# Kernel optimization log

Hardware: AMD Instinct MI355X
Metric: run time of the kernel (lower is better)

The kernel has to match this reference:

```python
import jax, jax.numpy as jnp
import numpy as np

T, B, I, H = 1024, 64, 256, 256


def setup_inputs() -> dict:
    key = jax.random.key(0)
    ks = jax.random.split(key, 7)
    s = 1.0 / np.sqrt(H)
    return {
        "x": jax.random.normal(ks[0], (T, B, I), jnp.float32),
        "U_w": jax.random.normal(ks[1], (H, I), jnp.float32) * s,
        "U_b": jax.random.normal(ks[2], (H,), jnp.float32) * s,
        "V_w": jax.random.normal(ks[3], (H, H), jnp.float32) * s,
        "Ua_w": jax.random.normal(ks[4], (H, H), jnp.float32) * s,
        "Va_w": jax.random.normal(ks[5], (H, H), jnp.float32) * s,
        "v": jax.random.normal(ks[6], (1, H), jnp.float32) * s,
    }


def reference(x, U_w, U_b, V_w, Ua_w, Va_w, v):
    # Unrolls MemRNN over the time axis of x: [T, B, I] -> [T, B, H].
    # Faithful to the torch module: st is the PRE-nonlinearity h at t=0;
    # for t>=1 st = memory[t-1] + ct (attention context), and memory stores
    # the POST-nonlinearity h.
    Tn = x.shape[0]
    vv = v[0]  # [H]
    # Precompute U(x_t) for all steps (input projection is step-independent).
    Ux = jnp.einsum('tbi,hi->tbh', x, U_w) + U_b  # [T, B, H]

    # t = 0: hidden is zeros, so V(hidden) = 0.
    st0 = Ux[0]                       # pre-nonlinearity state [B, H]
    h0 = jnp.tanh(st0)                # stored in memory
    mem0 = jnp.zeros((Tn,) + h0.shape, x.dtype).at[0].set(h0)
    # Incrementally maintain Ua(memory) so each step only projects the new h.
    uam0 = jnp.zeros_like(mem0).at[0].set(h0 @ Ua_w.T)

    tidx = jnp.arange(Tn)

    def step(carry, inp):
        mem, uam, st = carry
        t, Ux_t = inp
        valid = (tidx < t)[:, None]                       # [T, 1] mask over memory
        # Bahdanau scores over all past hidden states.
        e = jnp.einsum('tbh,h->tb', jnp.tanh(st @ Va_w.T + uam), vv)  # [T, B]
        e = jnp.where(valid, e, -jnp.inf)
        alphas = jax.nn.softmax(e, axis=0)                # softmax over time
        ct = jnp.einsum('tb,tbh->bh', alphas, mem)        # attention context
        last_h = jax.lax.dynamic_index_in_dim(mem, t - 1, 0, keepdims=False)
        st_new = last_h + ct
        h = jnp.tanh(Ux_t + st_new @ V_w.T)
        mem = mem.at[t].set(h)
        uam = uam.at[t].set(h @ Ua_w.T)
        return (mem, uam, st_new), h

    _, hs = jax.lax.scan(step, (mem0, uam0, st0), (tidx[1:], Ux[1:]))
    return jnp.concatenate([h0[None], hs], axis=0)  # [T, B, H]
```

## Files before the change

kernel.cpp:

```cpp
#include <hip/hip_runtime.h>
#include <hip/hip_fp16.h>

#define TT 1024
#define BB 64
#define HH 256
#define NQ 4
#define SL 64
#define NTH 1024
#define NW 16

#define MIR_BYTES (256ull * TT * SL * 2)
#define STW_BYTES (1ull * BB * HH * 4)
#define EP_BYTES  (1ull * BB * NQ * TT * 4)
#define BAR_BYTES ((BB * 32 + 32) * 4)
#define WS_NEED   (MIR_BYTES + STW_BYTES + EP_BYTES + BAR_BYTES)

__device__ __forceinline__ float tanh_fast(float xx) {
  float e = __expf(2.0f * xx);
  return 1.0f - 2.0f * __builtin_amdgcn_rcpf(e + 1.0f);
}

__device__ __forceinline__ float ld_cg(const float* p) {
  return __hip_atomic_load(p, __ATOMIC_RELAXED, __HIP_MEMORY_SCOPE_AGENT);
}
__device__ __forceinline__ void st_cg(float* p, float v) {
  __hip_atomic_store(p, v, __ATOMIC_RELAXED, __HIP_MEMORY_SCOPE_AGENT);
}

__device__ __forceinline__ void bar_post(int* cnt) {
  __syncthreads();
  if (threadIdx.x == 0)
    __hip_atomic_fetch_add(cnt, 1, __ATOMIC_RELEASE, __HIP_MEMORY_SCOPE_AGENT);
}
__device__ __forceinline__ void bar_wait(int* cnt, int* broken, int target) {
  if (threadIdx.x == 0) {
    long it = 0;
    while (__hip_atomic_load(cnt, __ATOMIC_RELAXED, __HIP_MEMORY_SCOPE_AGENT) < target) {
      if (__hip_atomic_load(broken, __ATOMIC_RELAXED, __HIP_MEMORY_SCOPE_AGENT)) break;
      if (++it > 5000000) {
        __hip_atomic_store(broken, 1, __ATOMIC_RELAXED, __HIP_MEMORY_SCOPE_AGENT);
        break;
      }
    }
  }
  __syncthreads();
}

#define RED16(a) { a += __shfl_xor(a, 1); a += __shfl_xor(a, 2); \
                   a += __shfl_xor(a, 4); a += __shfl_xor(a, 8); }

extern "C" __global__ void __launch_bounds__(NTH, 4)
memrnn_scan(const float* __restrict__ x, const float* __restrict__ U_w,
            const float* __restrict__ U_b, const float* __restrict__ V_w,
            const float* __restrict__ Ua_w, const float* __restrict__ Va_w,
            const float* __restrict__ vvec, float* __restrict__ out,
            char* __restrict__ wsb)
{
  const int blk  = blockIdx.x;
  const int b    = blk & 63;
  const int q    = blk >> 6;
  const int tid  = threadIdx.x;
  const int lane = tid & 63;
  const int wav  = tid >> 6;
  const int r    = tid >> 4;
  const int c    = tid & 15;
  const int gr   = q * SL + r;

  __half* mir = (__half*)wsb + (size_t)blk * TT * SL;
  float*  stw = (float*)(wsb + MIR_BYTES);
  float*  ep  = (float*)(wsb + MIR_BYTES + STW_BYTES);
  int* barbase = (int*)(wsb + MIR_BYTES + STW_BYTES + EP_BYTES);
  int* bar    = barbase + b * 32;
  int* broken = barbase + BB * 32;

  float wV[16], wUa[16], wVa[16], wU[16];
#pragma unroll
  for (int j = 0; j < 16; ++j) {
    const int i = j * 16 + c;
    wV[j]  = V_w [gr * HH + i];
    wUa[j] = Ua_w[gr * HH + i];
    wVa[j] = Va_w[gr * HH + i];
    wU[j]  = U_w [gr * HH + i];
  }
  const float bias = U_b[gr];

  __shared__ __half s_uam[TT * SL];
  __shared__ float2 s_av[SL];
  __shared__ float  s_vec[HH];
  __shared__ float  s_x[HH];
  __shared__ float  s_h[HH];
  __shared__ float  s_e[TT];
  __shared__ float  s_red[NW * SL];
  __shared__ float  s_d[NW];

  int tgt = 0;

  if (tid < HH) s_x[tid] = x[(size_t)b * HH + tid];
  __syncthreads();
  {
    float acc = 0.f;
#pragma unroll
    for (int j = 0; j < 16; ++j) acc += wU[j] * s_x[j * 16 + c];
    RED16(acc);
    if (c == 0) st_cg(&stw[b * HH + gr], acc + bias);
  }
  bar_post(bar); tgt += NQ; bar_wait(bar, broken, tgt);
  if (tid < HH) {
    const float sv = ld_cg(&stw[b * HH + tid]);
    s_vec[tid] = sv;
    s_h[tid]   = tanh_fast(sv);
  }
  __syncthreads();
  if (tid < SL) {
    const float h0 = s_h[q * SL + tid];
    st_cg(&out[(size_t)b * HH + q * SL + tid], h0);
    mir[tid] = __float2half(h0);
  }
  {
    float acca = 0.f, accu = 0.f;
#pragma unroll
    for (int j = 0; j < 16; ++j) {
      const int i = j * 16 + c;
      acca += wVa[j] * s_vec[i];
      accu += wUa[j] * s_h[i];
    }
    RED16(acca); RED16(accu);
    if (c == 0) {
      s_av[r] = make_float2(acca, vvec[gr]);
      s_uam[r] = __float2half(accu);
    }
  }
  __syncthreads();

  for (int t = 1; t < TT; ++t) {
    {
      float* epg = ep + ((size_t)(b * NQ + q)) * TT;
      for (int ci = wav; ci * SL < t; ci += NW) {
        const int t2 = ci * SL + lane;
        const int rb = t2 * SL;
        float p = 0.f;
#pragma unroll 8
        for (int h = 0; h < SL; ++h) {
          const float2 av = s_av[h];
          const float u = __half2float(s_uam[rb + (h ^ lane)]);
          p = fmaf(av.y, tanh_fast(av.x + u), p);
        }
        if (t2 < t) st_cg(&epg[t2], p);
      }
    }
    bar_post(bar); tgt += NQ; bar_wait(bar, broken, tgt);

    if (tid < t) {
      const float* e0 = ep + (size_t)b * NQ * TT + tid;
      s_e[tid] = ld_cg(e0) + ld_cg(e0 + TT) + ld_cg(e0 + 2 * TT) + ld_cg(e0 + 3 * TT);
    }
    __syncthreads();
    {
      float num = 0.f, den = 0.f;
#pragma unroll 4
      for (int t2 = wav; t2 < t; t2 += NW) {
        const float w = __expf(s_e[t2]);
        den += w;
        num = fmaf(w, __half2float(mir[(size_t)t2 * SL + lane]), num);
      }
      s_red[wav * SL + lane] = num;
      if (lane == 0) s_d[wav] = den;
    }
    __syncthreads();
    if (wav == 0) {
      float nt = 0.f, dt = 0.f;
#pragma unroll
      for (int w2 = 0; w2 < NW; ++w2) { nt += s_red[w2 * SL + lane]; dt += s_d[w2]; }
      const float ct  = nt / dt;
      const float stn = __half2float(mir[(size_t)(t - 1) * SL + lane]) + ct;
      st_cg(&stw[b * HH + q * SL + lane], stn);
    }
    float xv = 0.f;
    bar_post(bar); tgt += NQ;
    if (tid < HH) xv = x[((size_t)t * BB + b) * HH + tid];
    bar_wait(bar, broken, tgt);

    if (tid < HH) {
      s_x[tid]   = xv;
      s_vec[tid] = ld_cg(&stw[b * HH + tid]);
    }
    __syncthreads();
    {
      float acc = 0.f, acca = 0.f;
#pragma unroll
      for (int j = 0; j < 16; ++j) {
        const int i = j * 16 + c;
        const float sv = s_vec[i];
        acc  += wV[j] * sv + wU[j] * s_x[i];
        acca += wVa[j] * sv;
      }
      RED16(acc); RED16(acca);
      if (c == 0) {
        const float hv = tanh_fast(acc + bias);
        st_cg(&out[((size_t)t * BB + b) * HH + gr], hv);
        mir[(size_t)t * SL + r] = __float2half(hv);
        s_av[r].x = acca;
      }
    }
    if (t < TT - 1) {
      bar_post(bar); tgt += NQ; bar_wait(bar, broken, tgt);
      if (tid < HH) s_h[tid] = ld_cg(&out[((size_t)t * BB + b) * HH + tid]);
      __syncthreads();
      {
        float acc = 0.f;
#pragma unroll
        for (int j = 0; j < 16; ++j) acc += wUa[j] * s_h[j * 16 + c];
        RED16(acc);
        if (c == 0) s_uam[t * SL + (r ^ (t & 63))] = __float2half(acc);
      }
      __syncthreads();
    }
  }

  if (tid == 0 &&
      __hip_atomic_load(broken, __ATOMIC_RELAXED, __HIP_MEMORY_SCOPE_AGENT))
    st_cg(&out[0], 1.0e6f);
}

__global__ void ws_sentinel(float* out) { out[0] = 2.0e6f; }

extern "C" void kernel_launch(void* const* d_in, const int* in_sizes, int n_in,
                              void* d_out, int out_size, void* d_ws, size_t ws_size,
                              hipStream_t stream) {
  const float* x    = (const float*)d_in[0];
  const float* U_w  = (const float*)d_in[1];
  const float* U_b  = (const float*)d_in[2];
  const float* V_w  = (const float*)d_in[3];
  const float* Ua_w = (const float*)d_in[4];
  const float* Va_w = (const float*)d_in[5];
  const float* v    = (const float*)d_in[6];
  float* out = (float*)d_out;

  if (ws_size < WS_NEED) {
    ws_sentinel<<<1, 1, 0, stream>>>(out);
    return;
  }
  hipMemsetAsync((char*)d_ws + (MIR_BYTES + STW_BYTES + EP_BYTES), 0, BAR_BYTES, stream);
  memrnn_scan<<<dim3(BB * NQ), dim3(NTH), 0, stream>>>(
      x, U_w, U_b, V_w, Ua_w, Va_w, v, out, (char*)d_ws);
}
```

Baseline: 21.17 ms.

## Split Ua projection by input slice and overlap with score computation via per-quarter flags

Replaces the single counter barrier with per-quarter flag slots (aflag/bflag/pflag). The Ua projection now uses column-slice partial sums from each block's own hidden values, written to a global parts buffer. This removes the barrier that waited for all four quarters' h before computing uam. The score pass over old timesteps overlaps with waiting for those partials, and the newest timestep's score is computed separately. Tanh is rewritten via exp2 and a sigmoid identity with a precomputed v-sum, exp is moved into the s_e load, and the uam layout is transposed. These changes add more flag traffic and risk subtle ordering or precision issues.

Result: slower. 27.25 ms (+28.7%).

```diff
diff --git a/kernel.cpp b/kernel.cpp
--- a/kernel.cpp
+++ b/kernel.cpp
@@ -10,35 +10,49 @@
 #define NW 16
 
 #define MIR_BYTES (256ull * TT * SL * 2)
-#define STW_BYTES (1ull * BB * HH * 4)
-#define EP_BYTES  (1ull * BB * NQ * TT * 4)
-#define BAR_BYTES ((BB * 32 + 32) * 4)
-#define WS_NEED   (MIR_BYTES + STW_BYTES + EP_BYTES + BAR_BYTES)
+#define STW_OFF   (MIR_BYTES)
+#define EP_OFF    (STW_OFF + 1ull * BB * HH * 4)
+#define PARTS_OFF (EP_OFF + 1ull * BB * NQ * TT * 4)
+#define AF_OFF    (PARTS_OFF + 1ull * BB * NQ * HH * 4)
+#define BF_OFF    (AF_OFF + 1ull * BB * NQ * 32 * 4)
+#define PF_OFF    (BF_OFF + 1ull * BB * NQ * 32 * 4)
+#define BR_OFF    (PF_OFF + 1ull * BB * NQ * 32 * 4)
+#define WS_NEED   (BR_OFF + 128)
+
+#define PM 2.88539008178f
+
+#if __has_builtin(__builtin_amdgcn_exp2f)
+#define EXP2F(x) __builtin_amdgcn_exp2f(x)
+#else
+#define EXP2F(x) __expf(0.69314718056f * (x))
+#endif
 
 __device__ __forceinline__ float tanh_fast(float xx) {
   float e = __expf(2.0f * xx);
   return 1.0f - 2.0f * __builtin_amdgcn_rcpf(e + 1.0f);
 }
 
+#define AGT __HIP_MEMORY_SCOPE_AGENT
 __device__ __forceinline__ float ld_cg(const float* p) {
-  return __hip_atomic_load(p, __ATOMIC_RELAXED, __HIP_MEMORY_SCOPE_AGENT);
+  return __hip_atomic_load(p, __ATOMIC_RELAXED, AGT);
 }
 __device__ __forceinline__ void st_cg(float* p, float v) {
-  __hip_atomic_store(p, v, __ATOMIC_RELAXED, __HIP_MEMORY_SCOPE_AGENT);
-}
-
-__device__ __forceinline__ void bar_post(int* cnt) {
+  __hip_atomic_store(p, v, __ATOMIC_RELAXED, AGT);
+}
+
+__device__ __forceinline__ void post1(int* slot) {
   __syncthreads();
   if (threadIdx.x == 0)
-    __hip_atomic_fetch_add(cnt, 1, __ATOMIC_RELEASE, __HIP_MEMORY_SCOPE_AGENT);
-}
-__device__ __forceinline__ void bar_wait(int* cnt, int* broken, int target) {
-  if (threadIdx.x == 0) {
+    __hip_atomic_fetch_add(slot, 1, __ATOMIC_RELEASE, AGT);
+}
+__device__ __forceinline__ void wait4(int* base, int val, int* broken) {
+  if (threadIdx.x < 4) {
+    const int* f = base + threadIdx.x * 32;
     long it = 0;
-    while (__hip_atomic_load(cnt, __ATOMIC_RELAXED, __HIP_MEMORY_SCOPE_AGENT) < target) {
-      if (__hip_atomic_load(broken, __ATOMIC_RELAXED, __HIP_MEMORY_SCOPE_AGENT)) break;
+    while (__hip_atomic_load(f, __ATOMIC_RELAXED, AGT) < val) {
+      if (__hip_atomic_load(broken, __ATOMIC_RELAXED, AGT)) break;
       if (++it > 5000000) {
-        __hip_atomic_store(broken, 1, __ATOMIC_RELAXED, __HIP_MEMORY_SCOPE_AGENT);
+        __hip_atomic_store(broken, 1, __ATOMIC_RELAXED, AGT);
         break;
       }
     }
@@ -65,37 +79,42 @@
   const int r    = tid >> 4;
   const int c    = tid & 15;
   const int gr   = q * SL + r;
-
-  __half* mir = (__half*)wsb + (size_t)blk * TT * SL;
-  float*  stw = (float*)(wsb + MIR_BYTES);
-  float*  ep  = (float*)(wsb + MIR_BYTES + STW_BYTES);
-  int* barbase = (int*)(wsb + MIR_BYTES + STW_BYTES + EP_BYTES);
-  int* bar    = barbase + b * 32;
-  int* broken = barbase + BB * 32;
-
-  float wV[16], wUa[16], wVa[16], wU[16];
+  const int r2   = tid >> 2;
+  const int c2   = tid & 3;
+
+  __half* mir   = (__half*)wsb + (size_t)blk * TT * SL;
+  float*  stw   = (float*)(wsb + STW_OFF);
+  float*  ep    = (float*)(wsb + EP_OFF);
+  float*  parts = (float*)(wsb + PARTS_OFF);
+  int* aflag = (int*)(wsb + AF_OFF) + b * NQ * 32;
+  int* bflag = (int*)(wsb + BF_OFF) + b * NQ * 32;
+  int* pflag = (int*)(wsb + PF_OFF) + b * NQ * 32;
+  int* broken = (int*)(wsb + BR_OFF);
+
+  float wV[16], wVa[16], wU[16], wUa2[16];
 #pragma unroll
   for (int j = 0; j < 16; ++j) {
     const int i = j * 16 + c;
     wV[j]  = V_w [gr * HH + i];
-    wUa[j] = Ua_w[gr * HH + i];
     wVa[j] = Va_w[gr * HH + i];
     wU[j]  = U_w [gr * HH + i];
+    wUa2[j] = Ua_w[r2 * HH + q * SL + c2 * 16 + j];
   }
   const float bias = U_b[gr];
 
-  __shared__ __half s_uam[TT * SL];
-  __shared__ float2 s_av[SL];
-  __shared__ float  s_vec[HH];
-  __shared__ float  s_x[HH];
-  __shared__ float  s_h[HH];
-  __shared__ float  s_e[TT];
-  __shared__ float  s_red[NW * SL];
-  __shared__ float  s_d[NW];
-
-  int tgt = 0;
+  __shared__ __half  s_uam[SL * TT];
+  __shared__ float2  s_av[SL];
+  __shared__ float   s_e[TT];
+  __shared__ float   s_vec[HH];
+  __shared__ float   s_x[HH];
+  __shared__ float   s_hown[SL];
+  __shared__ float   s_red[NW * SL];
+  __shared__ float   s_d[NW];
+
+  float* epg = ep + (size_t)(b * NQ + q) * TT;
 
   if (tid < HH) s_x[tid] = x[(size_t)b * HH + tid];
+  if (tid < SL) s_av[tid] = make_float2(0.f, vvec[q * SL + tid]);
   __syncthreads();
   {
     float acc = 0.f;
@@ -104,64 +123,78 @@
     RED16(acc);
     if (c == 0) st_cg(&stw[b * HH + gr], acc + bias);
   }
-  bar_post(bar); tgt += NQ; bar_wait(bar, broken, tgt);
-  if (tid < HH) {
-    const float sv = ld_cg(&stw[b * HH + tid]);
-    s_vec[tid] = sv;
-    s_h[tid]   = tanh_fast(sv);
-  }
+  post1(bflag + q * 32);
+  float Vs = s_av[lane].y;
+  Vs += __shfl_xor(Vs, 1);  Vs += __shfl_xor(Vs, 2);  Vs += __shfl_xor(Vs, 4);
+  Vs += __shfl_xor(Vs, 8);  Vs += __shfl_xor(Vs, 16); Vs += __shfl_xor(Vs, 32);
+  wait4(bflag, 1, broken);
+  if (tid < HH) s_vec[tid] = ld_cg(&stw[b * HH + tid]);
   __syncthreads();
   if (tid < SL) {
-    const float h0 = s_h[q * SL + tid];
-    st_cg(&out[(size_t)b * HH + q * SL + tid], h0);
+    const float h0 = tanh_fast(s_vec[q * SL + tid]);
+    out[(size_t)b * HH + q * SL + tid] = h0;
     mir[tid] = __float2half(h0);
+    s_hown[tid] = h0;
   }
   {
-    float acca = 0.f, accu = 0.f;
-#pragma unroll
-    for (int j = 0; j < 16; ++j) {
-      const int i = j * 16 + c;
-      acca += wVa[j] * s_vec[i];
-      accu += wUa[j] * s_h[i];
-    }
-    RED16(acca); RED16(accu);
-    if (c == 0) {
-      s_av[r] = make_float2(acca, vvec[gr]);
-      s_uam[r] = __float2half(accu);
-    }
-  }
-  __syncthreads();
+    float acca = 0.f;
+#pragma unroll
+    for (int j = 0; j < 16; ++j) acca += wVa[j] * s_vec[j * 16 + c];
+    RED16(acca);
+    if (c == 0) s_av[r].x = PM * acca;
+  }
+  __syncthreads();
+  {
+    float pa = 0.f;
+#pragma unroll
+    for (int k = 0; k < 16; ++k) pa += wUa2[k] * s_hown[c2 * 16 + k];
+    pa += __shfl_xor(pa, 1); pa += __shfl_xor(pa, 2);
+    if (c2 == 0) st_cg(&parts[(size_t)(b * NQ + q) * HH + r2], pa);
+  }
+  post1(pflag + q * 32);
 
   for (int t = 1; t < TT; ++t) {
-    {
-      float* epg = ep + ((size_t)(b * NQ + q)) * TT;
-      for (int ci = wav; ci * SL < t; ci += NW) {
-        const int t2 = ci * SL + lane;
-        const int rb = t2 * SL;
-        float p = 0.f;
-#pragma unroll 8
-        for (int h = 0; h < SL; ++h) {
-          const float2 av = s_av[h];
-          const float u = __half2float(s_uam[rb + (h ^ lane)]);
-          p = fmaf(av.y, tanh_fast(av.x + u), p);
-        }
-        if (t2 < t) st_cg(&epg[t2], p);
-      }
-    }
-    bar_post(bar); tgt += NQ; bar_wait(bar, broken, tgt);
+    for (int ci = wav; ci * SL < t - 1; ci += NW) {
+      const int t2 = ci * SL + lane;
+      const __half* up = s_uam + ci * SL + lane;
+      float p2 = 0.f;
+#pragma unroll 16
+      for (int h = 0; h < SL; ++h) {
+        const float2 av = s_av[h];
+        const float uu = __half2float(up[h * TT]);
+        const float rr = __builtin_amdgcn_rcpf(1.f + EXP2F(av.x + uu));
+        p2 = fmaf(av.y, rr, p2);
+      }
+      if (t2 < t - 1) st_cg(&epg[t2], Vs - 2.f * p2);
+    }
+    wait4(pflag, t, broken);
+    if (tid < SL) {
+      const float* pp = parts + (size_t)b * NQ * HH + q * SL + tid;
+      const float u4 = ld_cg(pp) + ld_cg(pp + HH) + ld_cg(pp + 2 * HH) + ld_cg(pp + 3 * HH);
+      const float up_ = PM * u4;
+      s_uam[tid * TT + (t - 1)] = __float2half(up_);
+      const float2 av = s_av[tid];
+      float term = av.y * __builtin_amdgcn_rcpf(1.f + EXP2F(av.x + up_));
+      term += __shfl_xor(term, 1);  term += __shfl_xor(term, 2);  term += __shfl_xor(term, 4);
+      term += __shfl_xor(term, 8);  term += __shfl_xor(term, 16); term += __shfl_xor(term, 32);
+      if (tid == 0) st_cg(&epg[t - 1], Vs - 2.f * term);
+    }
+    post1(aflag + q * 32);
+    wait4(aflag, t, broken);
 
     if (tid < t) {
       const float* e0 = ep + (size_t)b * NQ * TT + tid;
-      s_e[tid] = ld_cg(e0) + ld_cg(e0 + TT) + ld_cg(e0 + 2 * TT) + ld_cg(e0 + 3 * TT);
+      s_e[tid] = __expf(ld_cg(e0) + ld_cg(e0 + TT) + ld_cg(e0 + 2 * TT) + ld_cg(e0 + 3 * TT));
     }
     __syncthreads();
     {
       float num = 0.f, den = 0.f;
-#pragma unroll 4
+      const __half* mq = mir + lane;
+#pragma unroll 8
       for (int t2 = wav; t2 < t; t2 += NW) {
-        const float w = __expf(s_e[t2]);
+        const float w = s_e[t2];
         den += w;
-        num = fmaf(w, __half2float(mir[(size_t)t2 * SL + lane]), num);
+        num = fmaf(w, __half2float(mq[(size_t)t2 * SL]), num);
       }
       s_red[wav * SL + lane] = num;
       if (lane == 0) s_d[wav] = den;
@@ -176,14 +209,11 @@
       st_cg(&stw[b * HH + q * SL + lane], stn);
     }
     float xv = 0.f;
-    bar_post(bar); tgt += NQ;
+    post1(bflag + q * 32);
     if (tid < HH) xv = x[((size_t)t * BB + b) * HH + tid];
-    bar_wait(bar, broken, tgt);
-
-    if (tid < HH) {
-      s_x[tid]   = xv;
-      s_vec[tid] = ld_cg(&stw[b * HH + tid]);
-    }
+    wait4(bflag, t + 1, broken);
+
+    if (tid < HH) { s_vec[tid] = ld_cg(&stw[b * HH + tid]); s_x[tid] = xv; }
     __syncthreads();
     {
       float acc = 0.f, acca = 0.f;
@@ -197,28 +227,24 @@
       RED16(acc); RED16(acca);
       if (c == 0) {
         const float hv = tanh_fast(acc + bias);
-        st_cg(&out[((size_t)t * BB + b) * HH + gr], hv);
+        out[((size_t)t * BB + b) * HH + gr] = hv;
         mir[(size_t)t * SL + r] = __float2half(hv);
-        s_av[r].x = acca;
+        s_hown[r] = hv;
+        s_av[r].x = PM * acca;
       }
     }
     if (t < TT - 1) {
-      bar_post(bar); tgt += NQ; bar_wait(bar, broken, tgt);
-      if (tid < HH) s_h[tid] = ld_cg(&out[((size_t)t * BB + b) * HH + tid]);
       __syncthreads();
-      {
-        float acc = 0.f;
-#pragma unroll
-        for (int j = 0; j < 16; ++j) acc += wUa[j] * s_h[j * 16 + c];
-        RED16(acc);
-        if (c == 0) s_uam[t * SL + (r ^ (t & 63))] = __float2half(acc);
-      }
-      __syncthreads();
-    }
-  }
-
-  if (tid == 0 &&
-      __hip_atomic_load(broken, __ATOMIC_RELAXED, __HIP_MEMORY_SCOPE_AGENT))
+      float pa = 0.f;
+#pragma unroll
+      for (int k = 0; k < 16; ++k) pa += wUa2[k] * s_hown[c2 * 16 + k];
+      pa += __shfl_xor(pa, 1); pa += __shfl_xor(pa, 2);
+      if (c2 == 0) st_cg(&parts[(size_t)(b * NQ + q) * HH + r2], pa);
+      post1(pflag + q * 32);
+    }
+  }
+
+  if (tid == 0 && __hip_atomic_load(broken, __ATOMIC_RELAXED, AGT))
     st_cg(&out[0], 1.0e6f);
 }
 
@@ -240,7 +266,7 @@
     ws_sentinel<<<1, 1, 0, stream>>>(out);
     return;
   }
-  hipMemsetAsync((char*)d_ws + (MIR_BYTES + STW_BYTES + EP_BYTES), 0, BAR_BYTES, stream);
+  hipMemsetAsync((char*)d_ws + AF_OFF, 0, (size_t)(BR_OFF - AF_OFF) + 128, stream);
   memrnn_scan<<<dim3(BB * NQ), dim3(NTH), 0, stream>>>(
       x, U_w, U_b, V_w, Ua_w, Va_w, v, out, (char*)d_ws);
 }
```
